# Performance work log

Measured on AMD Instinct MI355X. Metric: run time of the kernel, lower is better.

The kernel has to match this reference:

```python
import jax, jax.numpy as jnp
import numpy as np

B, L_IN, D = 4, 4096, 1024
R_MIN, R_MAX = 0.9, 0.999


def setup_inputs() -> dict:
    key = jax.random.key(0)
    k0, k1, k2 = jax.random.split(key, 3)
    inputs = jax.random.normal(k0, (B, L_IN, D), jnp.float32)
    Wi = jax.random.normal(k1, (2 * D, D), jnp.float32) / np.sqrt(D)
    bi = jnp.zeros((2 * D,), jnp.float32)
    Wo = jax.random.normal(k2, (D, 2 * D), jnp.float32) / np.sqrt(2 * D)
    bo = jnp.zeros((D,), jnp.float32)
    # LRU stable-ring initialization, exactly as in the torch module
    rng = np.random.default_rng(0)
    u1 = rng.random(D)
    u2 = rng.random(D)
    v_log = np.log(-0.5 * np.log(u1 * (R_MAX ** 2 - R_MIN ** 2) + R_MIN ** 2))
    theta_log = np.log(u2 * np.pi * 2)
    gamma_log = np.log(np.sqrt(1.0 - np.exp(-np.exp(v_log)) ** 2))
    params_log = jnp.asarray(np.stack([v_log, theta_log, gamma_log]), jnp.float32)
    return {"inputs": inputs, "Wi": Wi, "bi": bi, "Wo": Wo, "bo": bo,
            "params_log": params_log}


def _lru_forward(inputs, Wi, bi, Wo, bo, params_log):
    b, l_in, d = inputs.shape
    u = inputs @ Wi.T + bi                      # [B, L, 2D]
    v, theta, gamma = jnp.exp(params_log)       # each [D]
    # torch.view_as_complex: interleaved (real, imag) pairs along last dim
    uc = u.reshape(b, l_in, d, 2)
    x = jax.lax.complex(uc[..., 0], uc[..., 1])  # [B, L, D] complex64
    log2_L = int(np.ceil(np.log2(l_in)))
    L = 2 ** log2_L
    x = jnp.pad(x, ((0, 0), (0, L - l_in), (0, 0)))
    # Blelloch-style log-depth scan: x_t = lambda * x_{t-1} + u_t,
    # lambda = exp(-v + i*theta)
    for i in range(1, log2_L + 1):
        blk = 2 ** i
        xb = x.reshape(b * L // blk, blk, d)
        x1, x2 = xb[:, : blk // 2], xb[:, blk // 2:]
        pos = jnp.arange(1, blk // 2 + 1, dtype=jnp.float32)  # [blk/2]
        lambs = jnp.exp(jax.lax.complex(-pos[:, None] * v,
                                        pos[:, None] * theta))  # [blk/2, D]
        x2 = x2 + lambs * x1[:, -1:]
        x = jnp.concatenate([x1, x2], axis=1).reshape(b, L, d)
    x = x[:, :l_in] * gamma.astype(x.dtype)     # normalize, drop padding
    xr = jnp.concatenate([x.real, x.imag], axis=-1)  # [B, L, 2D]
    out = xr @ Wo.T + bo
    return jax.nn.relu(out)


def reference(inputs, Wi, bi, Wo, bo, params_log):
    return _lru_forward(inputs, Wi, bi, Wo, bo, params_log)
```

## Files before the change

kernel.cpp:

```cpp
#include <hip/hip_runtime.h>

#define BB 4
#define LL 4096
#define DD 1024
#define SS 64
#define TT 64
#define NCH 16

typedef __attribute__((ext_vector_type(4))) float  floatx4;
typedef __attribute__((ext_vector_type(8))) short  shortx8;
typedef __attribute__((ext_vector_type(8))) unsigned short ushortx8;

static __device__ __forceinline__ unsigned short f2bf(float f) {
    unsigned int u = __float_as_uint(f);
    u += 0x7fffu + ((u >> 16) & 1u);
    return (unsigned short)(u >> 16);
}
static __device__ __forceinline__ float bf2f(unsigned short h) {
    return __uint_as_float(((unsigned int)h) << 16);
}

#define NIN4 (BB * LL * DD / 4)
#define NWI4 (2 * DD * DD / 4)
#define NWO8 (DD * DD / 4)
__global__ void cast_all_kernel(const float4* __restrict__ s_in, ushort4* __restrict__ d_inb,
                                const float4* __restrict__ s_wi, ushort4* __restrict__ d_wib,
                                const float* __restrict__ s_wo, unsigned short* __restrict__ d_wob,
                                int* __restrict__ flags) {
    int i = blockIdx.x * blockDim.x + threadIdx.x;
    if (i < NCH * SS)
        __hip_atomic_store(&flags[i], 0, __ATOMIC_RELAXED, __HIP_MEMORY_SCOPE_AGENT);
    if (i < NIN4 + NWI4) {
        const float4* s; ushort4* d; int j;
        if (i < NIN4) { s = s_in; d = d_inb; j = i; }
        else          { s = s_wi; d = d_wib; j = i - NIN4; }
        float4 v = s[j];
        ushort4 o;
        o.x = f2bf(v.x); o.y = f2bf(v.y); o.z = f2bf(v.z); o.w = f2bf(v.w);
        d[j] = o;
    } else {
        int j = i - NIN4 - NWI4;
        int n  = j >> 8;
        int d0 = (j & 255) * 4;
        const float* rowp = s_wo + (size_t)n * (2 * DD);
        float4 re = *(const float4*)(rowp + d0);
        float4 im = *(const float4*)(rowp + DD + d0);
        ushortx8 o;
        o[0] = f2bf(re.x); o[1] = f2bf(im.x);
        o[2] = f2bf(re.y); o[3] = f2bf(im.y);
        o[4] = f2bf(re.z); o[5] = f2bf(im.z);
        o[6] = f2bf(re.w); o[7] = f2bf(im.w);
        *(ushortx8*)(d_wob + (size_t)n * (2 * DD) + 2 * d0) = o;
    }
}

template<int K, int NT, int EPI>
__global__ __launch_bounds__(512, 2)
void gemm256(const unsigned short* __restrict__ A,
             const unsigned short* __restrict__ B,
             const float* __restrict__ bias,
             void* __restrict__ Cp) {
    constexpr int N   = NT * 256;
    constexpr int NKT = K / 64;
    __shared__ __align__(16) short As[2][256 * 64];
    __shared__ __align__(16) short Bs[2][256 * 64];

    const int tid = threadIdx.x;
    const int blk = blockIdx.x;
    const int xcd = blk & 7;
    const int i2  = blk >> 3;
    const int tileM = ((i2 / NT) * 8 + xcd) * 256;
    const int tileN = (i2 % NT) * 256;

    const int lane   = tid & 63;
    const int wave   = tid >> 6;
    const int wave_m = wave >> 2;
    const int wave_n = wave & 3;
    const int r16    = lane & 15;
    const int quad   = lane >> 4;
    const int slotx  = r16 & 7;
    const int wmRow  = wave_m * 64 + r16;
    const int wnRow  = wave_n * 32 + r16;

    const int srow = tid >> 3;
    const int scol = ((tid & 7) ^ (srow & 7)) * 8;
    const int ldsChunkBase = (tid & ~63) * 8;
    const size_t aOff = (size_t)(tileM + srow) * K + scol;
    const size_t bOff = (size_t)(tileN + srow) * K + scol;

    floatx4 acc[8][4] = {};
    shortx8 af[4][2], bf0v[2][2], bf1v[2][2];

#define GLL(SRC, DST) __builtin_amdgcn_global_load_lds( \
        (const __attribute__((address_space(1))) void*)(SRC), \
        (__attribute__((address_space(3))) void*)(DST), 16, 0, 0)
#define STAGE_A(BUF, H, KT) do { \
    GLL(A + aOff + (size_t)((H) * 128) * K + (KT) * 64,      &As[BUF][(H) * 8192 + ldsChunkBase]); \
    GLL(A + aOff + (size_t)((H) * 128 + 64) * K + (KT) * 64, &As[BUF][(H) * 8192 + 4096 + ldsChunkBase]); \
} while (0)
#define STAGE_B(BUF, H, KT) do { \
    GLL(B + bOff + (size_t)((H) * 128) * K + (KT) * 64,      &Bs[BUF][(H) * 8192 + ldsChunkBase]); \
    GLL(B + bOff + (size_t)((H) * 128 + 64) * K + (KT) * 64, &Bs[BUF][(H) * 8192 + 4096 + ldsChunkBase]); \
} while (0)
#define LOAD_A(BUF, MH) do { \
    _Pragma("unroll") for (int il = 0; il < 4; ++il) \
    _Pragma("unroll") for (int kk = 0; kk < 2; ++kk) \
        af[il][kk] = *(const shortx8*)&As[BUF][((MH) * 128 + wmRow + il * 16) * 64 + ((kk * 4 + quad) ^ slotx) * 8]; \
} while (0)
#define LOAD_B(BUF, NH, DST) do { \
    _Pragma("unroll") for (int jl = 0; jl < 2; ++jl) \
    _Pragma("unroll") for (int kk = 0; kk < 2; ++kk) \
        DST[jl][kk] = *(const shortx8*)&Bs[BUF][((NH) * 128 + wnRow + jl * 16) * 64 + ((kk * 4 + quad) ^ slotx) * 8]; \
} while (0)
#define MFMAQ(MH, NH, BF) do { \
    __builtin_amdgcn_s_setprio(1); \
    _Pragma("unroll") for (int kk = 0; kk < 2; ++kk) \
    _Pragma("unroll") for (int il = 0; il < 4; ++il) \
    _Pragma("unroll") for (int jl = 0; jl < 2; ++jl) \
        acc[(MH) * 4 + il][(NH) * 2 + jl] = __builtin_amdgcn_mfma_f32_16x16x32_bf16( \
            af[il][kk], BF[jl][kk], acc[(MH) * 4 + il][(NH) * 2 + jl], 0, 0, 0); \
    __builtin_amdgcn_s_setprio(0); \
} while (0)
#define BAR()  __builtin_amdgcn_s_barrier()
#define LGKM0() asm volatile("s_waitcnt lgkmcnt(0)" ::: "memory")

    STAGE_A(0, 0, 0);
    STAGE_B(0, 0, 0);
    STAGE_B(0, 1, 0);
    STAGE_A(0, 1, 0);
    STAGE_A(1, 0, 1);
    STAGE_B(1, 1, 1);
    STAGE_A(1, 1, 1);
    asm volatile("s_waitcnt vmcnt(6)" ::: "memory");
    BAR();
    LOAD_A(0, 0);
    LOAD_B(0, 0, bf0v);

#pragma unroll 2
    for (int t = 0; t < NKT; ++t) {
        const int cb = t & 1;
        const int t1 = (t + 1 < NKT) ? t + 1 : NKT - 1;
        const int t2 = (t + 2 < NKT) ? t + 2 : NKT - 1;
        BAR();
        LGKM0();
        STAGE_B(cb ^ 1, 0, t1);
        MFMAQ(0, 0, bf0v);
        LOAD_B(cb, 1, bf1v);
        BAR();
        LGKM0();
        STAGE_A(cb, 0, t2);
        MFMAQ(0, 1, bf1v);
        LOAD_A(cb, 1);
        BAR();
        LGKM0();
        STAGE_B(cb, 1, t2);
        MFMAQ(1, 0, bf0v);
        asm volatile("s_waitcnt vmcnt(4)" ::: "memory");
        BAR();
        STAGE_A(cb, 1, t2);
        MFMAQ(1, 1, bf1v);
        LOAD_A(cb ^ 1, 0);
        LOAD_B(cb ^ 1, 0, bf0v);
    }
    asm volatile("s_waitcnt vmcnt(0) lgkmcnt(0)" ::: "memory");

#pragma unroll
    for (int i = 0; i < 8; ++i) {
        const int row0 = tileM + (i >> 2) * 128 + wave_m * 64 + (i & 3) * 16 + quad * 4;
#pragma unroll
        for (int j = 0; j < 4; ++j) {
            const int col = tileN + (j >> 1) * 128 + wave_n * 32 + (j & 1) * 16 + r16;
            const float bv = bias[col];
#pragma unroll
            for (int r = 0; r < 4; ++r) {
                float v = acc[i][j][r] + bv;
                if (EPI == 0) {
                    ((unsigned short*)Cp)[(size_t)(row0 + r) * N + col] = f2bf(v);
                } else {
                    ((float*)Cp)[(size_t)(row0 + r) * N + col] = fmaxf(v, 0.0f);
                }
            }
        }
    }
#undef GLL
#undef STAGE_A
#undef STAGE_B
#undef LOAD_A
#undef LOAD_B
#undef MFMAQ
#undef BAR
#undef LGKM0
}

__global__ __launch_bounds__(256, 4)
void scan_onepass(const unsigned short* __restrict__ u,
                  const float* __restrict__ plog,
                  unsigned long long* __restrict__ Epub,
                  int* __restrict__ flags,
                  unsigned short* __restrict__ xr) {
    __shared__ unsigned int wl[32][256];
    const int tid = threadIdx.x;
    const int d = blockIdx.x * 256 + tid;
    const int c = blockIdx.y, b = blockIdx.z;
    const int chain = b * (DD / 256) + blockIdx.x;

    unsigned int w[32];
    {
        const unsigned short* up = u + (size_t)(b * LL + c * TT) * (2 * DD) + 2 * d;
#pragma unroll
        for (int tl = 0; tl < 32; ++tl) { w[tl] = *(const unsigned int*)up; up += 2 * DD; }
#pragma unroll
        for (int tl = 0; tl < 32; ++tl) { wl[tl][tid] = *(const unsigned int*)up; up += 2 * DD; }
    }
    const float v  = expf(plog[d]);
    const float th = expf(plog[DD + d]);
    const float a  = expf(-v);
    const float lr = a * cosf(th), li = a * sinf(th);

    {
        float zr = 0.f, zi = 0.f;
#pragma unroll
        for (int tl = 0; tl < 32; ++tl) {
            float xv = bf2f((unsigned short)(w[tl] & 0xffffu));
            float yv = bf2f((unsigned short)(w[tl] >> 16));
            float t = lr * zr - li * zi + xv;
            zi = lr * zi + li * zr + yv;
            zr = t;
        }
#pragma unroll 8
        for (int tl = 0; tl < 32; ++tl) {
            unsigned int q = wl[tl][tid];
            float xv = bf2f((unsigned short)(q & 0xffffu));
            float yv = bf2f((unsigned short)(q >> 16));
            float t = lr * zr - li * zi + xv;
            zi = lr * zi + li * zr + yv;
            zr = t;
        }
        unsigned long long q = (unsigned long long)__float_as_uint(zr) |
                               ((unsigned long long)__float_as_uint(zi) << 32);
        __hip_atomic_store(&Epub[(size_t)c * (BB * DD) + b * DD + d], q,
                           __ATOMIC_RELAXED, __HIP_MEMORY_SCOPE_AGENT);
    }
    asm volatile("s_waitcnt vmcnt(0)" ::: "memory");
    __syncthreads();
    if (tid == 0)
        __hip_atomic_store(&flags[chain * SS + c], 1,
                           __ATOMIC_RELAXED, __HIP_MEMORY_SCOPE_AGENT);

    float yr = 0.f, yi = 0.f;
    if (c > 0) {
        const float aT = expf(-(float)TT * v);
        const float Lr = aT * cosf((float)TT * th), Li = aT * sinf((float)TT * th);
        const int fbase = chain * SS;
        if (tid == 0) {
            for (int j0 = 0; j0 < c; j0 += 8) {
                for (;;) {
                    int got = 0;
#pragma unroll
                    for (int k = 0; k < 8; ++k) {
                        got += (j0 + k >= c) ? 1 :
                            (__hip_atomic_load(&flags[fbase + j0 + k],
                                 __ATOMIC_RELAXED, __HIP_MEMORY_SCOPE_AGENT) != 0);
                    }
                    if (got == 8) break;
                    __builtin_amdgcn_s_sleep(8);
                }
            }
        }
        __syncthreads();
        const size_t pbase = (size_t)b * DD + d;
#define PLD(JJ) __hip_atomic_load(&Epub[(size_t)(JJ) * (BB * DD) + pbase], \
                                  __ATOMIC_RELAXED, __HIP_MEMORY_SCOPE_AGENT)
#define COMB(Q) do { \
        float er = __uint_as_float((unsigned int)(Q)); \
        float ei = __uint_as_float((unsigned int)((Q) >> 32)); \
        float t = Lr * yr - Li * yi + er; \
        yi = Lr * yi + Li * yr + ei; \
        yr = t; } while (0)
        int j = 0;
        for (; j + 4 <= c; j += 4) {
            unsigned long long q0 = PLD(j + 0), q1 = PLD(j + 1);
            unsigned long long q2 = PLD(j + 2), q3 = PLD(j + 3);
            COMB(q0); COMB(q1); COMB(q2); COMB(q3);
        }
        for (; j < c; ++j) { unsigned long long q = PLD(j); COMB(q); }
#undef PLD
#undef COMB
    }

    {
        const float g = expf(plog[2 * DD + d]);
        unsigned short* xp = xr + (size_t)(b * LL + c * TT) * (2 * DD) + 2 * d;
#pragma unroll
        for (int tl = 0; tl < 32; ++tl) {
            float xv = bf2f((unsigned short)(w[tl] & 0xffffu));
            float yv = bf2f((unsigned short)(w[tl] >> 16));
            float t = lr * yr - li * yi + xv;
            yi = lr * yi + li * yr + yv;
            yr = t;
            *(unsigned int*)xp = (unsigned int)f2bf(g * yr) |
                                 ((unsigned int)f2bf(g * yi) << 16);
            xp += 2 * DD;
        }
#pragma unroll 8
        for (int tl = 0; tl < 32; ++tl) {
            unsigned int q = wl[tl][tid];
            float xv = bf2f((unsigned short)(q & 0xffffu));
            float yv = bf2f((unsigned short)(q >> 16));
            float t = lr * yr - li * yi + xv;
            yi = lr * yi + li * yr + yv;
            yr = t;
            *(unsigned int*)xp = (unsigned int)f2bf(g * yr) |
                                 ((unsigned int)f2bf(g * yi) << 16);
            xp += 2 * DD;
        }
    }
}

extern "C" void kernel_launch(void* const* d_in, const int* in_sizes, int n_in,
                              void* d_out, int out_size, void* d_ws, size_t ws_size,
                              hipStream_t stream) {
    const float* inputs = (const float*)d_in[0];
    const float* Wi     = (const float*)d_in[1];
    const float* bi     = (const float*)d_in[2];
    const float* Wo     = (const float*)d_in[3];
    const float* bo     = (const float*)d_in[4];
    const float* plog   = (const float*)d_in[5];
    float* out = (float*)d_out;

    const size_t M = (size_t)BB * LL;
    unsigned short* u_bf  = (unsigned short*)d_ws;
    unsigned short* xr_bf = u_bf  + M * 2 * DD;
    unsigned short* in_bf = xr_bf + M * 2 * DD;
    unsigned short* Wi_bf = in_bf + M * DD;
    unsigned short* Wo_bf = Wi_bf + (size_t)2 * DD * DD;
    unsigned long long* Epub = (unsigned long long*)in_bf;
    int* flags = (int*)(Wo_bf + (size_t)2 * DD * DD);

    {
        int total = NIN4 + NWI4 + NWO8;
        cast_all_kernel<<<total / 256, 256, 0, stream>>>(
            (const float4*)inputs, (ushort4*)in_bf,
            (const float4*)Wi,     (ushort4*)Wi_bf,
            Wo,                    Wo_bf,
            flags);
    }

    gemm256<DD, 8, 0><<<(M / 256) * 8, 512, 0, stream>>>(
        in_bf, Wi_bf, bi, (void*)u_bf);

    scan_onepass<<<dim3(DD / 256, SS, BB), 256, 0, stream>>>(
        u_bf, plog, Epub, flags, xr_bf);

    gemm256<2 * DD, 4, 1><<<(M / 256) * 4, 512, 0, stream>>>(
        xr_bf, Wo_bf, bo, (void*)out);
}
```

Baseline: 295.0 us.

## Fuse fp32-to-bf16 input cast into first GEMM's A-tile staging

Removes the separate pass that converts the activations to bf16. The first GEMM now loads fp32 A tiles into registers, converts them to bf16, and stores them to shared memory, while B still uses direct global-to-LDS loads. This drops a full write and re-read of the bf16 input copy. The cost is doubled A bytes per GEMM tile load, extra VGPRs, and in-register conversion work inside the pipelined loop.

```diff
diff --git a/kernel.cpp b/kernel.cpp
--- a/kernel.cpp
+++ b/kernel.cpp
@@ -20,26 +20,21 @@
     return __uint_as_float(((unsigned int)h) << 16);
 }
 
-#define NIN4 (BB * LL * DD / 4)
 #define NWI4 (2 * DD * DD / 4)
 #define NWO8 (DD * DD / 4)
-__global__ void cast_all_kernel(const float4* __restrict__ s_in, ushort4* __restrict__ d_inb,
-                                const float4* __restrict__ s_wi, ushort4* __restrict__ d_wib,
-                                const float* __restrict__ s_wo, unsigned short* __restrict__ d_wob,
-                                int* __restrict__ flags) {
+__global__ void cast_wb_kernel(const float4* __restrict__ s_wi, ushort4* __restrict__ d_wib,
+                               const float* __restrict__ s_wo, unsigned short* __restrict__ d_wob,
+                               int* __restrict__ flags) {
     int i = blockIdx.x * blockDim.x + threadIdx.x;
     if (i < NCH * SS)
         __hip_atomic_store(&flags[i], 0, __ATOMIC_RELAXED, __HIP_MEMORY_SCOPE_AGENT);
-    if (i < NIN4 + NWI4) {
-        const float4* s; ushort4* d; int j;
-        if (i < NIN4) { s = s_in; d = d_inb; j = i; }
-        else          { s = s_wi; d = d_wib; j = i - NIN4; }
-        float4 v = s[j];
+    if (i < NWI4) {
+        float4 v = s_wi[i];
         ushort4 o;
         o.x = f2bf(v.x); o.y = f2bf(v.y); o.z = f2bf(v.z); o.w = f2bf(v.w);
-        d[j] = o;
+        d_wib[i] = o;
     } else {
-        int j = i - NIN4 - NWI4;
+        int j = i - NWI4;
         int n  = j >> 8;
         int d0 = (j & 255) * 4;
         const float* rowp = s_wo + (size_t)n * (2 * DD);
@@ -54,9 +49,9 @@
     }
 }
 
-template<int K, int NT, int EPI>
+template<int K, int NT, int EPI, int AF32>
 __global__ __launch_bounds__(512, 2)
-void gemm256(const unsigned short* __restrict__ A,
+void gemm256(const void* __restrict__ Ap,
              const unsigned short* __restrict__ B,
              const float* __restrict__ bias,
              void* __restrict__ Cp) {
@@ -64,6 +59,9 @@
     constexpr int NKT = K / 64;
     __shared__ __align__(16) short As[2][256 * 64];
     __shared__ __align__(16) short Bs[2][256 * 64];
+
+    const unsigned short* A  = (const unsigned short*)Ap;
+    const float*          Af = (const float*)Ap;
 
     const int tid = threadIdx.x;
     const int blk = blockIdx.x;
@@ -85,11 +83,13 @@
     const int srow = tid >> 3;
     const int scol = ((tid & 7) ^ (srow & 7)) * 8;
     const int ldsChunkBase = (tid & ~63) * 8;
+    const int ldsWr = tid * 8;
     const size_t aOff = (size_t)(tileM + srow) * K + scol;
     const size_t bOff = (size_t)(tileN + srow) * K + scol;
 
     floatx4 acc[8][4] = {};
     shortx8 af[4][2], bf0v[2][2], bf1v[2][2];
+    float4 a0_, a1_, a2_, a3_;
 
 #define GLL(SRC, DST) __builtin_amdgcn_global_load_lds( \
         (const __attribute__((address_space(1))) void*)(SRC), \
@@ -101,6 +101,21 @@
 #define STAGE_B(BUF, H, KT) do { \
     GLL(B + bOff + (size_t)((H) * 128) * K + (KT) * 64,      &Bs[BUF][(H) * 8192 + ldsChunkBase]); \
     GLL(B + bOff + (size_t)((H) * 128 + 64) * K + (KT) * 64, &Bs[BUF][(H) * 8192 + 4096 + ldsChunkBase]); \
+} while (0)
+#define AISSUE(H, KT) do { \
+    const float* ap_ = Af + aOff + (size_t)((H) * 128) * K + (KT) * 64; \
+    a0_ = *(const float4*)ap_;  a1_ = *(const float4*)(ap_ + 4); \
+    const float* ap2_ = ap_ + (size_t)64 * K; \
+    a2_ = *(const float4*)ap2_; a3_ = *(const float4*)(ap2_ + 4); \
+} while (0)
+#define AWRITE(BUF, H) do { \
+    shortx8 p0_, p1_; \
+    p0_[0]=(short)f2bf(a0_.x); p0_[1]=(short)f2bf(a0_.y); p0_[2]=(short)f2bf(a0_.z); p0_[3]=(short)f2bf(a0_.w); \
+    p0_[4]=(short)f2bf(a1_.x); p0_[5]=(short)f2bf(a1_.y); p0_[6]=(short)f2bf(a1_.z); p0_[7]=(short)f2bf(a1_.w); \
+    p1_[0]=(short)f2bf(a2_.x); p1_[1]=(short)f2bf(a2_.y); p1_[2]=(short)f2bf(a2_.z); p1_[3]=(short)f2bf(a2_.w); \
+    p1_[4]=(short)f2bf(a3_.x); p1_[5]=(short)f2bf(a3_.y); p1_[6]=(short)f2bf(a3_.z); p1_[7]=(short)f2bf(a3_.w); \
+    *(shortx8*)&As[BUF][(H) * 8192 + ldsWr]        = p0_; \
+    *(shortx8*)&As[BUF][(H) * 8192 + 4096 + ldsWr] = p1_; \
 } while (0)
 #define LOAD_A(BUF, MH) do { \
     _Pragma("unroll") for (int il = 0; il < 4; ++il) \
@@ -124,15 +139,28 @@
 #define BAR()  __builtin_amdgcn_s_barrier()
 #define LGKM0() asm volatile("s_waitcnt lgkmcnt(0)" ::: "memory")
 
-    STAGE_A(0, 0, 0);
-    STAGE_B(0, 0, 0);
-    STAGE_B(0, 1, 0);
-    STAGE_A(0, 1, 0);
-    STAGE_A(1, 0, 1);
-    STAGE_B(1, 1, 1);
-    STAGE_A(1, 1, 1);
-    asm volatile("s_waitcnt vmcnt(6)" ::: "memory");
-    BAR();
+    if constexpr (AF32) {
+        AISSUE(0, 0); AWRITE(0, 0);
+        AISSUE(1, 0); AWRITE(0, 1);
+        STAGE_B(0, 0, 0);
+        STAGE_B(0, 1, 0);
+        AISSUE(0, 1); AWRITE(1, 0);
+        AISSUE(1, 1); AWRITE(1, 1);
+        STAGE_B(1, 1, 1);
+        asm volatile("s_waitcnt vmcnt(2)" ::: "memory");
+        LGKM0();
+        BAR();
+    } else {
+        STAGE_A(0, 0, 0);
+        STAGE_B(0, 0, 0);
+        STAGE_B(0, 1, 0);
+        STAGE_A(0, 1, 0);
+        STAGE_A(1, 0, 1);
+        STAGE_B(1, 1, 1);
+        STAGE_A(1, 1, 1);
+        asm volatile("s_waitcnt vmcnt(6)" ::: "memory");
+        BAR();
+    }
     LOAD_A(0, 0);
     LOAD_B(0, 0, bf0v);
 
@@ -143,21 +171,24 @@
         const int t2 = (t + 2 < NKT) ? t + 2 : NKT - 1;
         BAR();
         LGKM0();
+        if constexpr (AF32) AISSUE(0, t2);
         STAGE_B(cb ^ 1, 0, t1);
         MFMAQ(0, 0, bf0v);
         LOAD_B(cb, 1, bf1v);
         BAR();
         LGKM0();
-        STAGE_A(cb, 0, t2);
+        if constexpr (AF32) AWRITE(cb, 0); else STAGE_A(cb, 0, t2);
         MFMAQ(0, 1, bf1v);
         LOAD_A(cb, 1);
         BAR();
         LGKM0();
+        if constexpr (AF32) AISSUE(1, t2);
         STAGE_B(cb, 1, t2);
         MFMAQ(1, 0, bf0v);
-        asm volatile("s_waitcnt vmcnt(4)" ::: "memory");
-        BAR();
-        STAGE_A(cb, 1, t2);
+        if constexpr (AF32) { asm volatile("s_waitcnt vmcnt(6)" ::: "memory"); }
+        else                { asm volatile("s_waitcnt vmcnt(4)" ::: "memory"); }
+        BAR();
+        if constexpr (AF32) AWRITE(cb, 1); else STAGE_A(cb, 1, t2);
         MFMAQ(1, 1, bf1v);
         LOAD_A(cb ^ 1, 0);
         LOAD_B(cb ^ 1, 0, bf0v);
@@ -185,6 +216,8 @@
 #undef GLL
 #undef STAGE_A
 #undef STAGE_B
+#undef AISSUE
+#undef AWRITE
 #undef LOAD_A
 #undef LOAD_B
 #undef MFMAQ
@@ -331,27 +364,21 @@
     const size_t M = (size_t)BB * LL;
     unsigned short* u_bf  = (unsigned short*)d_ws;
     unsigned short* xr_bf = u_bf  + M * 2 * DD;
-    unsigned short* in_bf = xr_bf + M * 2 * DD;
-    unsigned short* Wi_bf = in_bf + M * DD;
+    unsigned short* spare = xr_bf + M * 2 * DD;
+    unsigned short* Wi_bf = spare + M * DD;
     unsigned short* Wo_bf = Wi_bf + (size_t)2 * DD * DD;
-    unsigned long long* Epub = (unsigned long long*)in_bf;
+    unsigned long long* Epub = (unsigned long long*)spare;
     int* flags = (int*)(Wo_bf + (size_t)2 * DD * DD);
 
-    {
-        int total = NIN4 + NWI4 + NWO8;
-        cast_all_kernel<<<total / 256, 256, 0, stream>>>(
-            (const float4*)inputs, (ushort4*)in_bf,
-            (const float4*)Wi,     (ushort4*)Wi_bf,
-            Wo,                    Wo_bf,
-            flags);
-    }
-
-    gemm256<DD, 8, 0><<<(M / 256) * 8, 512, 0, stream>>>(
-        in_bf, Wi_bf, bi, (void*)u_bf);
+    cast_wb_kernel<<<(NWI4 + NWO8) / 256, 256, 0, stream>>>(
+        (const float4*)Wi, (ushort4*)Wi_bf, Wo, Wo_bf, flags);
+
+    gemm256<DD, 8, 0, 1><<<(M / 256) * 8, 512, 0, stream>>>(
+        (const void*)inputs, Wi_bf, bi, (void*)u_bf);
 
     scan_onepass<<<dim3(DD / 256, SS, BB), 256, 0, stream>>>(
         u_bf, plog, Epub, flags, xr_bf);
 
-    gemm256<2 * DD, 4, 1><<<(M / 256) * 4, 512, 0, stream>>>(
-        xr_bf, Wo_bf, bo, (void*)out);
-}
+    gemm256<2 * DD, 4, 1, 0><<<(M / 256) * 4, 512, 0, stream>>>(
+        (const void*)xr_bf, Wo_bf, bo, (void*)out);
+}
```

Result: slower. 342.6 us (+16.1%).
